# Kernel optimization log

Hardware: AMD Instinct MI355X
Metric: run time of the kernel (lower is better)

## Reference

```python
import jax, jax.numpy as jnp
import numpy as np

B, T, E = 128, 8, 52
S, R, L = 2048, 512, 4
VOCAB = 512


def setup_inputs() -> dict:
    key = jax.random.key(0)
    ks = jax.random.split(key, 16)
    enc_len = jax.random.randint(ks[5], (B,), 0, S, dtype=jnp.int32)
    enc_len = jnp.maximum(enc_len, 1)  # ragged lengths >= 1
    return {
        "featEmbed": jax.random.normal(ks[0], (B, T, E), jnp.float32),
        "labelsEmbed": jax.random.normal(ks[1], (B, T, E), jnp.float32),
        "encoder_outputs": jax.random.normal(ks[2], (B, S, R), jnp.float32),
        "h_n": jax.random.normal(ks[3], (B, R), jnp.float32),
        "mask": jax.random.randint(ks[4], (B, T), 0, 2, dtype=jnp.int32),
        "enc_len": enc_len,
        "emb_feat_table": jax.random.normal(ks[6], (VOCAB, E), jnp.float32) * 0.1,
        "W_fc_pool": jax.random.normal(ks[7], (L, R), jnp.float32) * (1.0 / np.sqrt(R)),
        "W_reg": jax.random.normal(ks[8], (L, R), jnp.float32) * (1.0 / np.sqrt(R)),
        "b_reg": jax.random.normal(ks[9], (L,), jnp.float32) * 0.01,
        "W_ih": jax.random.normal(ks[10], (3 * R, 2 * E), jnp.float32) * (1.0 / np.sqrt(2 * E)),
        "W_hh": jax.random.normal(ks[11], (3 * R, R), jnp.float32) * (1.0 / np.sqrt(R)),
        "b_ih": jax.random.normal(ks[12], (3 * R,), jnp.float32) * 0.01,
        "b_hh": jax.random.normal(ks[13], (3 * R,), jnp.float32) * 0.01,
    }


# label -> feature-vocab remap (dict d in original forward)
REMAP = jnp.array([175, 176, 44, 173], dtype=jnp.int32)


def _gru_cell(x, h, W_ih, W_hh, b_ih, b_hh):
    # PyTorch nn.GRUCell semantics
    gi = x @ W_ih.T + b_ih  # [B, 3R]
    gh = h @ W_hh.T + b_hh
    i_r, i_z, i_n = jnp.split(gi, 3, axis=1)
    h_r, h_z, h_nn = jnp.split(gh, 3, axis=1)
    r = jax.nn.sigmoid(i_r + h_r)
    z = jax.nn.sigmoid(i_z + h_z)
    n = jnp.tanh(i_n + r * h_nn)
    return (1.0 - z) * n + z * h


def reference(featEmbed, labelsEmbed, encoder_outputs, h_n, mask, enc_len,
              emb_feat_table, W_fc_pool, W_reg, b_reg, W_ih, W_hh, b_ih, b_hh):
    S_ = encoder_outputs.shape[1]
    # Ragged max-pool over valid encoder positions (replaces per-sample AdaptiveMaxPool1d loop)
    valid = jnp.arange(S_)[None, :] < enc_len[:, None]          # [B, S]
    neg = jnp.finfo(encoder_outputs.dtype).min
    code_pool = jnp.max(jnp.where(valid[:, :, None], encoder_outputs, neg), axis=1)  # [B, R]
    a = code_pool @ W_fc_pool.T                                  # [B, L]; constant over t

    def step(h, inp):
        x, bmi_t, m = inp                                        # [B,E], [B,E], [B]
        bmi_h = h @ W_reg.T + b_reg + a                          # [B, L]
        bmi_prob = jax.nn.sigmoid(bmi_h)
        bmi_label = jnp.argmax(bmi_prob, axis=1)                 # [B]
        label_dict = REMAP[bmi_label]                            # host-dict remap, vectorized
        bmi_label_enc = emb_feat_table[label_dict]               # [B, E]
        mf = m.astype(x.dtype)[:, None]
        bmi = bmi_t * mf + (1.0 - mf) * bmi_label_enc
        h_new = _gru_cell(jnp.concatenate([x, bmi], axis=1), h, W_ih, W_hh, b_ih, b_hh)
        return h_new, (bmi_label, bmi_prob, bmi_h, label_dict)

    xs = (jnp.swapaxes(featEmbed, 0, 1),    # [T,B,E]
          jnp.swapaxes(labelsEmbed, 0, 1),  # [T,B,E]
          mask.T)                            # [T,B]
    _, (dec_output, dec_prob, disc_input, kl_input) = jax.lax.scan(step, h_n, xs)
    L_ = dec_prob.shape[-1]
    # dec_output: [T,B] labels; dec_prob: [T,B,L]; disc_input: [T*B,L]; kl_input: [T*B]
    return dec_output, dec_prob, disc_input.reshape(-1, L_), kl_input.reshape(-1)
```

## Files before the change

### kernel.cpp

```cpp
#include <hip/hip_runtime.h>
#include <float.h>
#include <math.h>


#define B_ 128
#define T_ 8
#define E_ 52
#define S_ 2048
#define R_ 512
#define L_ 4
#define GR_ 1536
#define KX_ 104
#define NCHUNK 16
#define SCHUNK (S_ / NCHUNK)
#define NQ_ 154
#define XQ_ 26

__device__ __constant__ int c_remap[4] = {175, 176, 44, 173};

__device__ __forceinline__ float sigmoidf(float x) { return 1.0f / (1.0f + expf(-x)); }
__device__ __forceinline__ float dot4(float4 w, float4 x, float a) {
    a = fmaf(w.x, x.x, a);
    a = fmaf(w.y, x.y, a);
    a = fmaf(w.z, x.z, a);
    a = fmaf(w.w, x.w, a);
    return a;
}

__global__ void k_pool_pack(const float* __restrict__ enc, const int* __restrict__ enc_len,
                            float4* __restrict__ partial,
                            const float* __restrict__ Wih, const float* __restrict__ Whh,
                            float4* __restrict__ Wp) {
    int idx = blockIdx.x;
    int tid = threadIdx.x;
    if (idx >= NCHUNK * B_) {
        int qd = idx - NCHUNK * B_;
        #pragma unroll
        for (int i = 0; i < 4; ++i) {
            int rr = tid + 128 * i;
            #pragma unroll
            for (int g = 0; g < 3; ++g) {
                int row = g * 512 + rr;
                float4 v;
                if (qd < XQ_) v = *(const float4*)(Wih + (size_t)row * KX_ + 4 * qd);
                else          v = *(const float4*)(Whh + (size_t)row * R_  + 4 * (qd - XQ_));
                Wp[((size_t)qd * 3 + g) * 512 + rr] = v;
            }
        }
        return;
    }
    int c = idx & (NCHUNK - 1);
    int b = idx >> 4;
    int len = enc_len[b];
    int s0 = c * SCHUNK;
    int s1 = min(s0 + SCHUNK, len);
    float4 m = make_float4(-FLT_MAX, -FLT_MAX, -FLT_MAX, -FLT_MAX);
    const float4* base = (const float4*)(enc + (size_t)b * S_ * R_);
    for (int s = s0; s < s1; ++s) {
        float4 v = base[(size_t)s * (R_ / 4) + tid];
        m.x = fmaxf(m.x, v.x);
        m.y = fmaxf(m.y, v.y);
        m.z = fmaxf(m.z, v.z);
        m.w = fmaxf(m.w, v.w);
    }
    partial[((size_t)b * NCHUNK + c) * (R_ / 4) + tid] = m;
}

__global__ void k_pool_a(const float* __restrict__ partial, const float* __restrict__ W_fc,
                         float* __restrict__ a_out) {
    int b = blockIdx.x;
    int tid = threadIdx.x;
    __shared__ float cp[R_];
    for (int r = tid; r < R_; r += 256) {
        float m = -FLT_MAX;
        const float* p = partial + (size_t)b * NCHUNK * R_ + r;
        #pragma unroll
        for (int c = 0; c < NCHUNK; ++c) m = fmaxf(m, p[c * R_]);
        cp[r] = m;
    }
    __syncthreads();
    float p0 = 0.f, p1 = 0.f, p2 = 0.f, p3 = 0.f;
    for (int r = tid; r < R_; r += 256) {
        float v = cp[r];
        p0 = fmaf(v, W_fc[0 * R_ + r], p0);
        p1 = fmaf(v, W_fc[1 * R_ + r], p1);
        p2 = fmaf(v, W_fc[2 * R_ + r], p2);
        p3 = fmaf(v, W_fc[3 * R_ + r], p3);
    }
    #pragma unroll
    for (int off = 32; off > 0; off >>= 1) {
        p0 += __shfl_down(p0, off);
        p1 += __shfl_down(p1, off);
        p2 += __shfl_down(p2, off);
        p3 += __shfl_down(p3, off);
    }
    __shared__ float red[4][4];
    int wv = tid >> 6, lane = tid & 63;
    if (lane == 0) { red[wv][0] = p0; red[wv][1] = p1; red[wv][2] = p2; red[wv][3] = p3; }
    __syncthreads();
    if (tid < 4) {
        a_out[b * L_ + tid] = red[0][tid] + red[1][tid] + red[2][tid] + red[3][tid];
    }
}

__global__ void __launch_bounds__(1024, 1) k_step(
        const float* __restrict__ h, const float* __restrict__ W_reg,
        const float* __restrict__ b_reg, const float* __restrict__ a_vec,
        const float* __restrict__ featEmbed, const float* __restrict__ labelsEmbed,
        const int* __restrict__ mask, const float* __restrict__ emb_table,
        const float4* __restrict__ Wp, const float* __restrict__ b_ih,
        const float* __restrict__ b_hh,
        int t, float* __restrict__ h_out, float* __restrict__ out) {
    int tid = threadIdx.x;
    int lane = tid & 63;
    int w = tid >> 6;
    int b0 = blockIdx.y * 8;
    int rrl = lane & 31;
    int bh = lane >> 5;
    int rr = blockIdx.x * 32 + rrl;

    __shared__ __align__(16) float xs[8][KX_];
    __shared__ __align__(16) float hs[8][R_];
    __shared__ float red[8][64][17];

    if (w >= 8) {
        int bi = w - 8;
        const float4* src = (const float4*)(h + (size_t)(b0 + bi) * R_);
        float4* dst = (float4*)hs[bi];
        dst[lane] = src[lane];
        dst[lane + 64] = src[lane + 64];
    }

    if (w < 8) {
        int bp = b0 + w;
        const float* hb = h + (size_t)bp * R_;
        float p0 = 0.f, p1 = 0.f, p2 = 0.f, p3 = 0.f;
        #pragma unroll
        for (int r = lane; r < R_; r += 64) {
            float v = hb[r];
            p0 = fmaf(v, W_reg[r], p0);
            p1 = fmaf(v, W_reg[512 + r], p1);
            p2 = fmaf(v, W_reg[1024 + r], p2);
            p3 = fmaf(v, W_reg[1536 + r], p3);
        }
        #pragma unroll
        for (int off = 32; off > 0; off >>= 1) {
            p0 += __shfl_down(p0, off);
            p1 += __shfl_down(p1, off);
            p2 += __shfl_down(p2, off);
            p3 += __shfl_down(p3, off);
        }
        p0 = __shfl(p0, 0); p1 = __shfl(p1, 0); p2 = __shfl(p2, 0); p3 = __shfl(p3, 0);
        float bh_[4];
        bh_[0] = p0 + b_reg[0] + a_vec[bp * 4 + 0];
        bh_[1] = p1 + b_reg[1] + a_vec[bp * 4 + 1];
        bh_[2] = p2 + b_reg[2] + a_vec[bp * 4 + 2];
        bh_[3] = p3 + b_reg[3] + a_vec[bp * 4 + 3];
        float pr[4];
        #pragma unroll
        for (int l = 0; l < 4; ++l) pr[l] = sigmoidf(bh_[l]);
        int best = 0;
        float bv = pr[0];
        #pragma unroll
        for (int l = 1; l < 4; ++l) {
            if (pr[l] > bv) { bv = pr[l]; best = l; }
        }
        int ld = c_remap[best];
        if (blockIdx.x == 0 && lane == 0) {
            out[t * B_ + bp] = (float)best;
            #pragma unroll
            for (int l = 0; l < 4; ++l) {
                out[1024 + (t * B_ + bp) * 4 + l] = pr[l];
                out[5120 + (t * B_ + bp) * 4 + l] = bh_[l];
            }
            out[9216 + t * B_ + bp] = (float)ld;
        }
        if (lane < E_) {
            xs[w][lane] = featEmbed[bp * (T_ * E_) + t * E_ + lane];
            int m = mask[bp * T_ + t];
            xs[w][E_ + lane] = m ? labelsEmbed[bp * (T_ * E_) + t * E_ + lane]
                                 : emb_table[ld * E_ + lane];
        }
    }
    __syncthreads();

    float acc[16];
    #pragma unroll
    for (int j = 0; j < 16; ++j) acc[j] = 0.f;

    int q0 = (NQ_ * w) >> 4;
    int q1 = (NQ_ * (w + 1)) >> 4;
    const float4* wp0 = Wp + (size_t)q0 * 1536 + rr;

    int xe = min(q1, XQ_);
    #pragma unroll 2
    for (int qd = q0; qd < xe; ++qd) {
        float4 wr = wp0[0];
        float4 wz = wp0[512];
        float4 wn = wp0[1024];
        wp0 += 1536;
        #pragma unroll
        for (int i = 0; i < 4; ++i) {
            float4 xv = *(const float4*)&xs[bh * 4 + i][4 * qd];
            acc[0 + i] = dot4(wr, xv, acc[0 + i]);
            acc[4 + i] = dot4(wz, xv, acc[4 + i]);
            acc[8 + i] = dot4(wn, xv, acc[8 + i]);
        }
    }
    int hq0 = max(q0, XQ_);
    #pragma unroll 2
    for (int qd = hq0; qd < q1; ++qd) {
        float4 wr = wp0[0];
        float4 wz = wp0[512];
        float4 wn = wp0[1024];
        wp0 += 1536;
        int hq = 4 * (qd - XQ_);
        #pragma unroll
        for (int i = 0; i < 4; ++i) {
            float4 xv = *(const float4*)&hs[bh * 4 + i][hq];
            acc[0 + i]  = dot4(wr, xv, acc[0 + i]);
            acc[4 + i]  = dot4(wz, xv, acc[4 + i]);
            acc[12 + i] = dot4(wn, xv, acc[12 + i]);
        }
    }

    if (w >= 8) {
        float* d = red[w - 8][lane];
        #pragma unroll
        for (int j = 0; j < 16; ++j) d[j] = acc[j];
    }
    __syncthreads();
    if (w < 8) {
        const float* s = red[w][lane];
        #pragma unroll
        for (int j = 0; j < 16; ++j) acc[j] += s[j];
    }
    if (w >= 4 && w < 8) {
        float* d = red[w][lane];
        #pragma unroll
        for (int j = 0; j < 16; ++j) d[j] = acc[j];
    }
    __syncthreads();
    if (w < 4) {
        const float* s = red[w + 4][lane];
        #pragma unroll
        for (int j = 0; j < 16; ++j) acc[j] += s[j];
    }
    if (w >= 2 && w < 4) {
        float* d = red[w][lane];
        #pragma unroll
        for (int j = 0; j < 16; ++j) d[j] = acc[j];
    }
    __syncthreads();
    if (w < 2) {
        const float* s = red[w + 2][lane];
        #pragma unroll
        for (int j = 0; j < 16; ++j) acc[j] += s[j];
    }
    if (w == 1) {
        float* d = red[1][lane];
        #pragma unroll
        for (int j = 0; j < 16; ++j) d[j] = acc[j];
    }
    __syncthreads();
    if (w == 0) {
        const float* s = red[1][lane];
        #pragma unroll
        for (int j = 0; j < 16; ++j) acc[j] += s[j];
        float bir = b_ih[rr],        bhr = b_hh[rr];
        float biz = b_ih[512 + rr],  bhz = b_hh[512 + rr];
        float bin = b_ih[1024 + rr], bhn = b_hh[1024 + rr];
        #pragma unroll
        for (int i = 0; i < 4; ++i) {
            int bi = bh * 4 + i;
            float r = sigmoidf(acc[0 + i] + bir + bhr);
            float z = sigmoidf(acc[4 + i] + biz + bhz);
            float n = tanhf(acc[8 + i] + bin + r * (acc[12 + i] + bhn));
            h_out[(size_t)(b0 + bi) * R_ + rr] = (1.0f - z) * n + z * hs[bi][rr];
        }
    }
}

extern "C" void kernel_launch(void* const* d_in, const int* in_sizes, int n_in,
                              void* d_out, int out_size, void* d_ws, size_t ws_size,
                              hipStream_t stream) {
    const float* featEmbed   = (const float*)d_in[0];
    const float* labelsEmbed = (const float*)d_in[1];
    const float* enc         = (const float*)d_in[2];
    const float* h_n         = (const float*)d_in[3];
    const int*   mask        = (const int*)d_in[4];
    const int*   enc_len     = (const int*)d_in[5];
    const float* emb_table   = (const float*)d_in[6];
    const float* W_fc        = (const float*)d_in[7];
    const float* W_reg       = (const float*)d_in[8];
    const float* b_reg       = (const float*)d_in[9];
    const float* W_ih        = (const float*)d_in[10];
    const float* W_hh        = (const float*)d_in[11];
    const float* b_ih        = (const float*)d_in[12];
    const float* b_hh        = (const float*)d_in[13];
    float* out = (float*)d_out;

    float* ws      = (float*)d_ws;
    float* partial = ws;
    float* Wp      = partial + B_ * NCHUNK * R_;
    float* h0      = Wp + NQ_ * 3 * R_ * 4;
    float* h1      = h0 + B_ * R_;
    float* a_vec   = h1 + B_ * R_;

    k_pool_pack<<<dim3(NCHUNK * B_ + NQ_), 128, 0, stream>>>(
        enc, enc_len, (float4*)partial, W_ih, W_hh, (float4*)Wp);
    k_pool_a<<<B_, 256, 0, stream>>>(partial, W_fc, a_vec);

    const float* hcur = h_n;
    for (int t = 0; t < T_; ++t) {
        float* hnext = (t & 1) ? h1 : h0;
        k_step<<<dim3(R_ / 32, B_ / 8), 1024, 0, stream>>>(
            hcur, W_reg, b_reg, a_vec, featEmbed, labelsEmbed, mask, emb_table,
            (const float4*)Wp, b_ih, b_hh, t, hnext, out);
        hcur = hnext;
    }
}
```

Measured before the change: 765.4 us.

## Share packed GRU weights between wavefront halves via cross-lane shuffles

In the GRU step kernel, each half-wavefront now loads the packed weight float4s for only one k-quad of each pair, and the two halves swap them with xor-32 shuffles. The old code had both halves load the same weights. This halves global/L2 weight traffic per wave but adds shuffle instructions. The k-range split across the 16 waves is changed to fixed pairs of quads, 5 or 4 pairs per wave. Pairs are assumed not to straddle the x/h boundary at quad 26.

```diff
diff --git a/kernel.cpp b/kernel.cpp
--- a/kernel.cpp
+++ b/kernel.cpp
@@ -25,6 +25,14 @@
     a = fmaf(w.z, x.z, a);
     a = fmaf(w.w, x.w, a);
     return a;
+}
+__device__ __forceinline__ float4 shfl_xor32(float4 v) {
+    float4 r;
+    r.x = __shfl_xor(v.x, 32);
+    r.y = __shfl_xor(v.y, 32);
+    r.z = __shfl_xor(v.z, 32);
+    r.w = __shfl_xor(v.w, 32);
+    return r;
 }
 
 __global__ void k_pool_pack(const float* __restrict__ enc, const int* __restrict__ enc_len,
@@ -116,7 +124,8 @@
     int w = tid >> 6;
     int b0 = blockIdx.y * 8;
     int rrl = lane & 31;
-    int bh = lane >> 5;
+    int half = lane >> 5;
+    int bh = half;
     int rr = blockIdx.x * 32 + rrl;
 
     __shared__ __align__(16) float xs[8][KX_];
@@ -188,39 +197,51 @@
     #pragma unroll
     for (int j = 0; j < 16; ++j) acc[j] = 0.f;
 
-    int q0 = (NQ_ * w) >> 4;
-    int q1 = (NQ_ * (w + 1)) >> 4;
-    const float4* wp0 = Wp + (size_t)q0 * 1536 + rr;
-
-    int xe = min(q1, XQ_);
+    int npair = (w <= 12) ? 5 : 4;
+    int ex = (w >= 14) ? (w - 13) : 0;
+    int q0 = 10 * w - 2 * ex;
+    const float4* WpB = Wp + rr;
+
     #pragma unroll 2
-    for (int qd = q0; qd < xe; ++qd) {
-        float4 wr = wp0[0];
-        float4 wz = wp0[512];
-        float4 wn = wp0[1024];
-        wp0 += 1536;
-        #pragma unroll
-        for (int i = 0; i < 4; ++i) {
-            float4 xv = *(const float4*)&xs[bh * 4 + i][4 * qd];
-            acc[0 + i] = dot4(wr, xv, acc[0 + i]);
-            acc[4 + i] = dot4(wz, xv, acc[4 + i]);
-            acc[8 + i] = dot4(wn, xv, acc[8 + i]);
-        }
-    }
-    int hq0 = max(q0, XQ_);
-    #pragma unroll 2
-    for (int qd = hq0; qd < q1; ++qd) {
-        float4 wr = wp0[0];
-        float4 wz = wp0[512];
-        float4 wn = wp0[1024];
-        wp0 += 1536;
-        int hq = 4 * (qd - XQ_);
-        #pragma unroll
-        for (int i = 0; i < 4; ++i) {
-            float4 xv = *(const float4*)&hs[bh * 4 + i][hq];
-            acc[0 + i]  = dot4(wr, xv, acc[0 + i]);
-            acc[4 + i]  = dot4(wz, xv, acc[4 + i]);
-            acc[12 + i] = dot4(wn, xv, acc[12 + i]);
+    for (int p = 0; p < npair; ++p) {
+        int qa = q0 + 2 * p;
+        int qown = qa + half;
+        int qoth = qa + 1 - half;
+        const float4* wb = WpB + (size_t)qown * 1536;
+        float4 wg0 = wb[0];
+        float4 wg1 = wb[512];
+        float4 wg2 = wb[1024];
+        float4 vg0 = shfl_xor32(wg0);
+        float4 vg1 = shfl_xor32(wg1);
+        float4 vg2 = shfl_xor32(wg2);
+        if (qa < XQ_) {
+            int co = 4 * qown, cx = 4 * qoth;
+            #pragma unroll
+            for (int i = 0; i < 4; ++i) {
+                int bi = (half << 2) + i;
+                float4 xo = *(const float4*)&xs[bi][co];
+                float4 xx = *(const float4*)&xs[bi][cx];
+                acc[0 + i] = dot4(wg0, xo, acc[0 + i]);
+                acc[0 + i] = dot4(vg0, xx, acc[0 + i]);
+                acc[4 + i] = dot4(wg1, xo, acc[4 + i]);
+                acc[4 + i] = dot4(vg1, xx, acc[4 + i]);
+                acc[8 + i] = dot4(wg2, xo, acc[8 + i]);
+                acc[8 + i] = dot4(vg2, xx, acc[8 + i]);
+            }
+        } else {
+            int co = 4 * (qown - XQ_), cx = 4 * (qoth - XQ_);
+            #pragma unroll
+            for (int i = 0; i < 4; ++i) {
+                int bi = (half << 2) + i;
+                float4 xo = *(const float4*)&hs[bi][co];
+                float4 xx = *(const float4*)&hs[bi][cx];
+                acc[0 + i]  = dot4(wg0, xo, acc[0 + i]);
+                acc[0 + i]  = dot4(vg0, xx, acc[0 + i]);
+                acc[4 + i]  = dot4(wg1, xo, acc[4 + i]);
+                acc[4 + i]  = dot4(vg1, xx, acc[4 + i]);
+                acc[12 + i] = dot4(wg2, xo, acc[12 + i]);
+                acc[12 + i] = dot4(vg2, xx, acc[12 + i]);
+            }
         }
     }
 
```

Result: no change. 772.7 us (+1.0%).
